# Performance work log

Hardware: AMD Instinct MI355X
Metric: run time of the kernel (lower is better)

The kernel has to match this reference:

```python
import jax, jax.numpy as jnp
import numpy as np

NUM_HEADS = 16

def setup_inputs() -> dict:
    key = jax.random.key(0)
    ks = jax.random.split(key, 11)
    B, S, D = 4, 1024, 1024
    M = 128
    hd = D // NUM_HEADS
    s = 0.02
    return {
        'x':  jax.random.normal(ks[0], (B, S, D), jnp.float32),
        'Wq': jax.random.normal(ks[1], (D, D), jnp.float32) * s,
        'bq': jax.random.normal(ks[2], (D,), jnp.float32) * s,
        'Wk': jax.random.normal(ks[3], (D, D), jnp.float32) * s,
        'bk': jax.random.normal(ks[4], (D,), jnp.float32) * s,
        'Wv': jax.random.normal(ks[5], (D, D), jnp.float32) * s,
        'bv': jax.random.normal(ks[6], (D,), jnp.float32) * s,
        'Wo': jax.random.normal(ks[7], (D, D), jnp.float32) * s,
        'bo': jax.random.normal(ks[8], (D,), jnp.float32) * s,
        'rel_k': jax.random.normal(ks[9], (2 * M + 1, hd), jnp.float32),
        'rel_v': jax.random.normal(ks[10], (2 * M + 1, hd), jnp.float32),
    }

def reference(x, Wq, bq, Wk, bk, Wv, bv, Wo, bo, rel_k, rel_v):
    B, S, D = x.shape
    H = NUM_HEADS
    hd = D // H
    M = (rel_k.shape[0] - 1) // 2

    def proj(W, b):
        # torch nn.Linear: x @ W.T + b, then split heads -> [B,H,S,hd]
        return (x @ W.T + b).reshape(B, S, H, hd).transpose(0, 2, 1, 3)

    q = proj(Wq, bq)
    k = proj(Wk, bk)
    v = proj(Wv, bv)

    # relative position index matrix [S,S]: clip(j - i, -M, M) + M
    r = jnp.arange(S)
    idx = jnp.clip(r[None, :] - r[:, None], -M, M) + M
    rpk = rel_k[idx]  # [S,S,hd] (equivalent to one-hot matmul lookup)
    rpv = rel_v[idx]  # [S,S,hd]

    content = jnp.einsum('bhqd,bhkd->bhqk', q, k)
    relative = jnp.einsum('bhqd,qkd->bhqk', q, rpk)
    scores = (content + relative) / jnp.sqrt(jnp.float32(hd))
    w = jax.nn.softmax(scores, axis=-1)  # [B,H,S,S]

    out = jnp.einsum('bhqk,bhkd->bhqd', w, v) + jnp.einsum('bhqk,qkd->bhqd', w, rpv)
    out = out.transpose(0, 2, 1, 3).reshape(B, S, D)
    return out @ Wo.T + bo
```

## Files before the change

### kernel.cpp

```cpp
#include <hip/hip_runtime.h>
#include <hip/hip_bf16.h>
#include <math.h>

#define SEQ 1024
#define NH 16
#define HD 64
#define DM 1024
#define MWIN 128
#define RR 257

typedef __attribute__((ext_vector_type(8))) short bf16x8;
typedef __attribute__((ext_vector_type(4))) float f32x4;

__device__ __forceinline__ unsigned short f2b_bits(float f) {
  return __builtin_bit_cast(unsigned short, __float2bfloat16(f));
}
__device__ __forceinline__ float b2f(unsigned short u) {
  return __uint_as_float(((unsigned int)u) << 16);
}
__device__ __forceinline__ void gl16(const void* g, void* l) {
  __builtin_amdgcn_global_load_lds(
      (const __attribute__((address_space(1))) unsigned int*)g,
      (__attribute__((address_space(3))) unsigned int*)l, 16, 0, 0);
}

__global__ __launch_bounds__(256) void prep_conv(const float* __restrict__ x,
                                                 const float* __restrict__ w0,
                                                 const float* __restrict__ w1,
                                                 const float* __restrict__ w2,
                                                 const float* __restrict__ w3,
                                                 const float* __restrict__ rk,
                                                 const float* __restrict__ rv,
                                                 unsigned short* __restrict__ xb,
                                                 unsigned short* __restrict__ wb,
                                                 unsigned short* __restrict__ relkb,
                                                 unsigned short* __restrict__ relvtb) {
  const int bid = blockIdx.x, t = threadIdx.x;
  if (bid < 4096) {
    int i = bid * 256 + t;
    float4 v = ((const float4*)x)[i];
    ushort4 o;
    o.x = f2b_bits(v.x); o.y = f2b_bits(v.y); o.z = f2b_bits(v.z); o.w = f2b_bits(v.w);
    ((ushort4*)xb)[i] = o;
  } else if (bid < 8192) {
    int idx = (bid - 4096) * 256 + t;
    const int m = idx >> 18, local = idx & 262143;
    const float* src = m == 0 ? w0 : (m == 1 ? w1 : (m == 2 ? w2 : w3));
    float4 v = ((const float4*)src)[local];
    ushort4 o;
    o.x = f2b_bits(v.x); o.y = f2b_bits(v.y); o.z = f2b_bits(v.z); o.w = f2b_bits(v.w);
    ((ushort4*)wb)[idx] = o;
  } else if (bid < 8288) {
    int idx = (bid - 8192) * 256 + t;
    int r = idx >> 6;
    int rs = r > 256 ? 256 : r;
    relkb[idx] = f2b_bits(rk[rs * HD + (idx & 63)]);
  } else {
    int idx = (bid - 8288) * 256 + t;
    if (idx < 64 * 288) {
      int d = idx / 288, r = idx % 288;
      relvtb[idx] = (r < RR) ? f2b_bits(rv[(size_t)r * HD + d]) : (unsigned short)0;
    }
  }
}

__global__ __launch_bounds__(256) void qkv_gemm(const unsigned short* __restrict__ A,
                                                const unsigned short* __restrict__ Bw,
                                                const float* __restrict__ bq,
                                                const float* __restrict__ bk,
                                                const float* __restrict__ bv,
                                                unsigned short* __restrict__ Qo,
                                                unsigned short* __restrict__ Ko,
                                                unsigned short* __restrict__ Vo) {
  __shared__ unsigned short As[128 * 32];
  __shared__ unsigned short Bs[128 * 32];
  const int t = threadIdx.x;
  const int lane = t & 63;
  const int wave = t >> 6;
  const int wr = wave >> 1, wc = wave & 1;
  const int lrow = lane & 15, lk = lane >> 4;
  const int m0 = blockIdx.x * 128, n0 = blockIdx.y * 128;

  const int mat = n0 >> 10;
  const float* bias = mat == 0 ? bq : (mat == 1 ? bk : bv);
  unsigned short* Co = mat == 0 ? Qo : (mat == 1 ? Ko : Vo);
  const float scale = mat == 0 ? 0.125f : 1.0f;

  const unsigned short* Ag = A + (size_t)m0 * DM;
  const unsigned short* Bg = Bw + (size_t)n0 * DM;
  const int r0 = t >> 2, r1 = (t + 256) >> 2;
  const int c0 = (t & 3) << 3;

  f32x4 acc[4][4] = {};

  for (int k0 = 0; k0 < DM; k0 += 32) {
    __syncthreads();
    gl16(Ag + (size_t)r0 * DM + k0 + c0, &As[t * 8]);
    gl16(Bg + (size_t)r0 * DM + k0 + c0, &Bs[t * 8]);
    gl16(Ag + (size_t)r1 * DM + k0 + c0, &As[(t + 256) * 8]);
    gl16(Bg + (size_t)r1 * DM + k0 + c0, &Bs[(t + 256) * 8]);
    __syncthreads();
    bf16x8 af[4], bfr[4];
#pragma unroll
    for (int i = 0; i < 4; ++i)
      af[i] = *(const bf16x8*)&As[(wr * 64 + i * 16 + lrow) * 32 + lk * 8];
#pragma unroll
    for (int j = 0; j < 4; ++j)
      bfr[j] = *(const bf16x8*)&Bs[(wc * 64 + j * 16 + lrow) * 32 + lk * 8];
#pragma unroll
    for (int i = 0; i < 4; ++i)
#pragma unroll
      for (int j = 0; j < 4; ++j)
        acc[i][j] = __builtin_amdgcn_mfma_f32_16x16x32_bf16(af[i], bfr[j], acc[i][j], 0, 0, 0);
  }

  float bvv[4];
#pragma unroll
  for (int j = 0; j < 4; ++j) bvv[j] = bias[(n0 & 1023) + wc * 64 + j * 16 + lrow];

#pragma unroll
  for (int i = 0; i < 4; ++i) {
#pragma unroll
    for (int j = 0; j < 4; ++j) {
      const int nl = (n0 & 1023) + wc * 64 + j * 16 + lrow;
      const int h = nl >> 6, d = nl & 63;
#pragma unroll
      for (int r = 0; r < 4; ++r) {
        const int m = m0 + wr * 64 + i * 16 + lk * 4 + r;
        const int b = m >> 10, s = m & 1023;
        float v = (acc[i][j][r] + bvv[j]) * scale;
        Co[((size_t)(b * NH + h) * SEQ + s) * HD + d] = f2b_bits(v);
      }
    }
  }
}

template<int MODE>
__global__ __launch_bounds__(256) void mfma_gemm(const unsigned short* __restrict__ A,
                                                 const unsigned short* __restrict__ B,
                                                 const float* __restrict__ bias,
                                                 float* __restrict__ Cf,
                                                 unsigned short* __restrict__ Cb,
                                                 int K) {
  __shared__ unsigned short As[128 * 32];
  __shared__ unsigned short Bs[128 * 32];
  const int t = threadIdx.x;
  const int lane = t & 63;
  const int wave = t >> 6;
  const int wr = wave >> 1, wc = wave & 1;
  const int lrow = lane & 15, lk = lane >> 4;
  const int m0 = blockIdx.x * 128, n0 = blockIdx.y * 128;

  const unsigned short* Ag = A + (size_t)m0 * K;
  const unsigned short* Bg = B + (size_t)n0 * K;
  const int r0 = t >> 2, r1 = (t + 256) >> 2;
  const int c0 = (t & 3) << 3;

  f32x4 acc[4][4] = {};

  for (int k0 = 0; k0 < K; k0 += 32) {
    __syncthreads();
    gl16(Ag + (size_t)r0 * K + k0 + c0, &As[t * 8]);
    gl16(Bg + (size_t)r0 * K + k0 + c0, &Bs[t * 8]);
    gl16(Ag + (size_t)r1 * K + k0 + c0, &As[(t + 256) * 8]);
    gl16(Bg + (size_t)r1 * K + k0 + c0, &Bs[(t + 256) * 8]);
    __syncthreads();
    bf16x8 af[4], bfr[4];
#pragma unroll
    for (int i = 0; i < 4; ++i)
      af[i] = *(const bf16x8*)&As[(wr * 64 + i * 16 + lrow) * 32 + lk * 8];
#pragma unroll
    for (int j = 0; j < 4; ++j)
      bfr[j] = *(const bf16x8*)&Bs[(wc * 64 + j * 16 + lrow) * 32 + lk * 8];
#pragma unroll
    for (int i = 0; i < 4; ++i)
#pragma unroll
      for (int j = 0; j < 4; ++j)
        acc[i][j] = __builtin_amdgcn_mfma_f32_16x16x32_bf16(af[i], bfr[j], acc[i][j], 0, 0, 0);
  }

  float bvv[4];
  if (MODE == 1) {
#pragma unroll
    for (int j = 0; j < 4; ++j) bvv[j] = bias[n0 + wc * 64 + j * 16 + lrow];
  }
#pragma unroll
  for (int i = 0; i < 4; ++i) {
#pragma unroll
    for (int j = 0; j < 4; ++j) {
      const int n = n0 + wc * 64 + j * 16 + lrow;
#pragma unroll
      for (int r = 0; r < 4; ++r) {
        const int m = m0 + wr * 64 + i * 16 + lk * 4 + r;
        float v = acc[i][j][r];
        if (MODE == 1) {
          Cf[(size_t)m * DM + n] = v + bvv[j];
        } else {
          if (n < RR) Cb[(size_t)m * RR + n] = f2b_bits(v);
        }
      }
    }
  }
}

#define FLASH_LDS_BYTES 126976

__global__ __launch_bounds__(512) void flash_mfma(
    const unsigned short* __restrict__ Qb,
    const unsigned short* __restrict__ Kb,
    const unsigned short* __restrict__ Vb,
    const unsigned short* __restrict__ qrb,
    const unsigned short* __restrict__ relvT,
    unsigned short* __restrict__ attnb) {
  extern __shared__ char smem[];
  unsigned short* Ks = (unsigned short*)smem;
  unsigned short (*VT)[144]    = (unsigned short(*)[144])(smem + 16384);
  unsigned short (*Ps)[16][72] = (unsigned short(*)[16][72])(smem + 34816);
  unsigned short (*wrs)[288]   = (unsigned short(*)[288])(smem + 53248);

  const int t = threadIdx.x;
  const int lane = t & 63;
  const int w = t >> 6;
  const int lq = lane & 15;
  const int g  = lane >> 4;
  const int bh = blockIdx.y;
  const int q0 = blockIdx.x * 128;
  const int qw0 = q0 + w * 16;

  const unsigned short* Qp = Qb + (size_t)bh * SEQ * HD;
  const unsigned short* Kp = Kb + (size_t)bh * SEQ * HD;
  const unsigned short* Vp = Vb + (size_t)bh * SEQ * HD;

  {
    unsigned int* wz = (unsigned int*)(smem + 53248);
    for (int i = t; i < 18432; i += 512) wz[i] = 0u;
  }

  bf16x8 aq[2];
  aq[0] = *(const bf16x8*)(Qp + (size_t)(qw0 + lq) * HD + g * 8);
  aq[1] = *(const bf16x8*)(Qp + (size_t)(qw0 + lq) * HD + 32 + g * 8);

  const size_t qrow0 = ((size_t)bh * SEQ + qw0 + g * 4) * RR;
  float bq0[4], bq256[4];
#pragma unroll
  for (int rr = 0; rr < 4; ++rr) {
    bq0[rr]   = b2f(qrb[qrow0 + (size_t)rr * RR]);
    bq256[rr] = b2f(qrb[qrow0 + (size_t)rr * RR + 256]);
  }

  float l[4] = {}, accL[4] = {}, accR[4] = {};
  f32x4 out1[4] = {};

  const int sv = 2 * lane;
  const int dvv = w * 8;
  bf16x8 v00 = *(const bf16x8*)(Vp + (size_t)sv * HD + dvv);
  bf16x8 v10 = *(const bf16x8*)(Vp + (size_t)(sv + 1) * HD + dvv);

  for (int kt = 0; kt < 8; ++kt) {
    const int k0 = kt * 128;
    __syncthreads();

#pragma unroll
    for (int u = 0; u < 2; ++u) {
      const int ch = t + u * 512;
      const int row = ch >> 3;
      const int src = (row << 3) | ((ch & 7) ^ (row & 7));
      gl16(Kp + (size_t)k0 * HD + src * 8, &Ks[ch * 8]);
    }
#pragma unroll
    for (int j = 0; j < 8; ++j) {
      *(unsigned int*)&VT[dvv + j][sv] =
          (unsigned short)v00[j] | ((unsigned int)(unsigned short)v10[j] << 16);
    }

    const int dh0 = k0 - qw0, dh1 = dh0 + 64;
    const int cls0 = dh0 <= -192 ? 0 : (dh0 >= 144 ? 1 : 2);
    const int cls1 = dh1 <= -192 ? 0 : (dh1 >= 144 ? 1 : 2);
    float bias0[4][4], bias1[4][4];
    if (cls0 == 2) {
      const int dbase = dh0 + lq - g * 4;
#pragma unroll
      for (int j = 0; j < 4; ++j)
#pragma unroll
        for (int rr = 0; rr < 4; ++rr) {
          int delta = dbase + j * 16 - rr;
          int r = delta < -MWIN ? 0 : (delta > MWIN ? 256 : delta + MWIN);
          bias0[j][rr] = b2f(qrb[qrow0 + (size_t)rr * RR + r]);
        }
    }
    if (cls1 == 2) {
      const int dbase = dh1 + lq - g * 4;
#pragma unroll
      for (int j = 0; j < 4; ++j)
#pragma unroll
        for (int rr = 0; rr < 4; ++rr) {
          int delta = dbase + j * 16 - rr;
          int r = delta < -MWIN ? 0 : (delta > MWIN ? 256 : delta + MWIN);
          bias1[j][rr] = b2f(qrb[qrow0 + (size_t)rr * RR + r]);
        }
    }
    __syncthreads();

    if (kt < 7) {
      const unsigned short* Vn = Vp + (size_t)(k0 + 128) * HD + dvv;
      v00 = *(const bf16x8*)(Vn + (size_t)sv * HD);
      v10 = *(const bf16x8*)(Vn + (size_t)(sv + 1) * HD);
    }

#pragma unroll
    for (int h = 0; h < 2; ++h) {
      const int dh = h == 0 ? dh0 : dh1;
      const int cls = h == 0 ? cls0 : cls1;
      const float (*bias)[4] = h == 0 ? bias0 : bias1;

      f32x4 sc[4] = {};
#pragma unroll
      for (int j = 0; j < 4; ++j) {
        const int row = h * 64 + j * 16 + lq;
#pragma unroll
        for (int kk = 0; kk < 2; ++kk) {
          const int ch = (kk * 4 + g) ^ (lq & 7);
          bf16x8 bk = *(const bf16x8*)&Ks[row * 64 + ch * 8];
          sc[j] = __builtin_amdgcn_mfma_f32_16x16x32_bf16(aq[kk], bk, sc[j], 0, 0, 0);
        }
      }

      float wvf[4][4], ssum[4] = {};
      if (cls == 2) {
#pragma unroll
        for (int j = 0; j < 4; ++j)
#pragma unroll
          for (int rr = 0; rr < 4; ++rr) {
            float wv = __expf(sc[j][rr] + bias[j][rr]);
            wvf[j][rr] = wv; ssum[rr] += wv;
          }
        const int dbase = dh + lq - g * 4;
#pragma unroll
        for (int j = 0; j < 4; ++j)
#pragma unroll
          for (int rr = 0; rr < 4; ++rr) {
            const unsigned short ub = f2b_bits(wvf[j][rr]);
            Ps[w][g * 4 + rr][j * 16 + lq] = ub;
            const int delta = dbase + j * 16 - rr;
            if (delta <= -MWIN)      accL[rr] += wvf[j][rr];
            else if (delta >= MWIN)  accR[rr] += wvf[j][rr];
            else                     wrs[w * 16 + g * 4 + rr][delta + MWIN] = ub;
          }
      } else {
        const float* bb = cls == 0 ? bq0 : bq256;
#pragma unroll
        for (int j = 0; j < 4; ++j)
#pragma unroll
          for (int rr = 0; rr < 4; ++rr) {
            float wv = __expf(sc[j][rr] + bb[rr]);
            wvf[j][rr] = wv; ssum[rr] += wv;
            Ps[w][g * 4 + rr][j * 16 + lq] = f2b_bits(wv);
          }
#pragma unroll
        for (int rr = 0; rr < 4; ++rr) {
          if (cls == 0) accL[rr] += ssum[rr]; else accR[rr] += ssum[rr];
        }
      }

#pragma unroll
      for (int rr = 0; rr < 4; ++rr) {
        float s0 = ssum[rr];
#pragma unroll
        for (int o = 1; o < 16; o <<= 1) s0 += __shfl_xor(s0, o);
        l[rr] += s0;
      }

      bf16x8 pa[2];
      pa[0] = *(const bf16x8*)&Ps[w][lq][g * 8];
      pa[1] = *(const bf16x8*)&Ps[w][lq][32 + g * 8];
#pragma unroll
      for (int jd = 0; jd < 4; ++jd) {
        const int vrow = jd * 16 + lq;
#pragma unroll
        for (int kk = 0; kk < 2; ++kk) {
          bf16x8 vb = *(const bf16x8*)&VT[vrow][h * 64 + kk * 32 + g * 8];
          out1[jd] = __builtin_amdgcn_mfma_f32_16x16x32_bf16(pa[kk], vb, out1[jd], 0, 0, 0);
        }
      }
    }
  }

#pragma unroll
  for (int rr = 0; rr < 4; ++rr) {
    float sL = accL[rr], sR = accR[rr];
#pragma unroll
    for (int o = 1; o < 16; o <<= 1) { sL += __shfl_xor(sL, o); sR += __shfl_xor(sR, o); }
    if (lq == 0) {
      wrs[w * 16 + g * 4 + rr][0]   = f2b_bits(sL);
      wrs[w * 16 + g * 4 + rr][256] = f2b_bits(sR);
    }
  }
  __syncthreads();

  f32x4 out2[4] = {};
#pragma unroll
  for (int kk = 0; kk < 9; ++kk) {
    bf16x8 pa2 = *(const bf16x8*)&wrs[w * 16 + lq][kk * 32 + g * 8];
#pragma unroll
    for (int jd = 0; jd < 4; ++jd) {
      bf16x8 vb = *(const bf16x8*)(relvT + (size_t)(jd * 16 + lq) * 288 + kk * 32 + g * 8);
      out2[jd] = __builtin_amdgcn_mfma_f32_16x16x32_bf16(pa2, vb, out2[jd], 0, 0, 0);
    }
  }

  const int b = bh >> 4, h = bh & 15;
#pragma unroll
  for (int jd = 0; jd < 4; ++jd)
#pragma unroll
    for (int rr = 0; rr < 4; ++rr) {
      const int s = qw0 + g * 4 + rr;
      const int d = jd * 16 + lq;
      float vout = (out1[jd][rr] + out2[jd][rr]) / l[rr];
      attnb[(size_t)(b * SEQ + s) * DM + h * HD + d] = f2b_bits(vout);
    }
}

extern "C" void kernel_launch(void* const* d_in, const int* in_sizes, int n_in,
                              void* d_out, int out_size, void* d_ws, size_t ws_size,
                              hipStream_t stream) {
  const float* x     = (const float*)d_in[0];
  const float* Wq    = (const float*)d_in[1];
  const float* bq    = (const float*)d_in[2];
  const float* Wk    = (const float*)d_in[3];
  const float* bk    = (const float*)d_in[4];
  const float* Wv    = (const float*)d_in[5];
  const float* bv    = (const float*)d_in[6];
  const float* Wo    = (const float*)d_in[7];
  const float* bo    = (const float*)d_in[8];
  const float* rel_k = (const float*)d_in[9];
  const float* rel_v = (const float*)d_in[10];
  float* out = (float*)d_out;

  unsigned short* us    = (unsigned short*)d_ws;
  unsigned short* qrb   = us;
  unsigned short* xb    = us + 16842752;
  unsigned short* attnb = xb;
  unsigned short* Wqb   = xb + 4194304;
  unsigned short* Wob   = Wqb + 3145728;
  unsigned short* Qbf   = Wob + 1048576;
  unsigned short* Kbb   = Qbf + 4194304;
  unsigned short* Vbb   = Kbb + 4194304;
  unsigned short* relkb = Vbb + 4194304;
  unsigned short* relvtb= relkb + 24576;

  prep_conv<<<8360, 256, 0, stream>>>(x, Wq, Wk, Wv, Wo, rel_k, rel_v,
                                      xb, Wqb, relkb, relvtb);

  qkv_gemm<<<dim3(32, 24), 256, 0, stream>>>(xb, Wqb, bq, bk, bv, Qbf, Kbb, Vbb);

  mfma_gemm<2><<<dim3(512, 3), 256, 0, stream>>>(Qbf, relkb, nullptr, nullptr, qrb, HD);

  (void)hipFuncSetAttribute(reinterpret_cast<const void*>(flash_mfma),
                            hipFuncAttributeMaxDynamicSharedMemorySize,
                            FLASH_LDS_BYTES);
  flash_mfma<<<dim3(8, 64), 512, FLASH_LDS_BYTES, stream>>>(Qbf, Kbb, Vbb, qrb, relvtb, attnb);

  mfma_gemm<1><<<dim3(32, 8), 256, 0, stream>>>(attnb, Wob, bo, out, nullptr, DM);
}
```

Baseline: 240.9 us.

## Prefetch relative bias one tile ahead, compute row sums via MFMA, remap blocks to XCDs

The flash attention kernel now gathers the relative-position bias values for the next key tile one iteration ahead into a double-buffered register array, so their global latency overlaps with the current tile's compute. The per-row softmax denominator is no longer reduced with 16-lane shuffles; it is accumulated by an extra MFMA of the probability tile against a vector of ones. Blocks are remapped so each XCD handles a contiguous group of heads, which is meant to improve L2 reuse of K/V. The final normalisation uses a reciprocal multiply instead of division. The trade-off is higher register pressure from full unrolling and the prefetch buffers, plus row sums that now come from the bf16-rounded probabilities.

```diff
diff --git a/kernel.cpp b/kernel.cpp
--- a/kernel.cpp
+++ b/kernel.cpp
@@ -205,6 +205,29 @@
 
 #define FLASH_LDS_BYTES 126976
 
+#define GATHER(KT, BUF)                                                        \
+  {                                                                            \
+    const int dg0 = (KT) * 128 - qw0, dg1 = dg0 + 64;                          \
+    if (dg0 > -192 && dg0 < 144) {                                             \
+      const int dbase = dg0 + lq - g * 4;                                      \
+      _Pragma("unroll") for (int j = 0; j < 4; ++j)                            \
+      _Pragma("unroll") for (int rr = 0; rr < 4; ++rr) {                       \
+        int delta = dbase + j * 16 - rr;                                       \
+        int r = delta < -MWIN ? 0 : (delta > MWIN ? 256 : delta + MWIN);       \
+        nb[BUF][0][j][rr] = qrb[qrow0 + (size_t)rr * RR + r];                  \
+      }                                                                        \
+    }                                                                          \
+    if (dg1 > -192 && dg1 < 144) {                                             \
+      const int dbase = dg1 + lq - g * 4;                                      \
+      _Pragma("unroll") for (int j = 0; j < 4; ++j)                            \
+      _Pragma("unroll") for (int rr = 0; rr < 4; ++rr) {                       \
+        int delta = dbase + j * 16 - rr;                                       \
+        int r = delta < -MWIN ? 0 : (delta > MWIN ? 256 : delta + MWIN);       \
+        nb[BUF][1][j][rr] = qrb[qrow0 + (size_t)rr * RR + r];                  \
+      }                                                                        \
+    }                                                                          \
+  }
+
 __global__ __launch_bounds__(512) void flash_mfma(
     const unsigned short* __restrict__ Qb,
     const unsigned short* __restrict__ Kb,
@@ -223,8 +246,11 @@
   const int w = t >> 6;
   const int lq = lane & 15;
   const int g  = lane >> 4;
-  const int bh = blockIdx.y;
-  const int q0 = blockIdx.x * 128;
+
+  const int id  = blockIdx.x + blockIdx.y * 8;
+  const int xcd = id & 7, j2 = id >> 3;
+  const int bh  = xcd * 8 + (j2 & 7);
+  const int q0  = (j2 >> 3) * 128;
   const int qw0 = q0 + w * 16;
 
   const unsigned short* Qp = Qb + (size_t)bh * SEQ * HD;
@@ -248,14 +274,22 @@
     bq256[rr] = b2f(qrb[qrow0 + (size_t)rr * RR + 256]);
   }
 
-  float l[4] = {}, accL[4] = {}, accR[4] = {};
-  f32x4 out1[4] = {};
+  bf16x8 vone;
+#pragma unroll
+  for (int i = 0; i < 8; ++i) vone[i] = (short)0x3F80;
+
+  float accL[4] = {}, accR[4] = {};
+  f32x4 out1[4] = {}, lacc = {};
 
   const int sv = 2 * lane;
   const int dvv = w * 8;
   bf16x8 v00 = *(const bf16x8*)(Vp + (size_t)sv * HD + dvv);
   bf16x8 v10 = *(const bf16x8*)(Vp + (size_t)(sv + 1) * HD + dvv);
 
+  unsigned short nb[2][2][4][4];
+  GATHER(0, 0);
+
+#pragma unroll
   for (int kt = 0; kt < 8; ++kt) {
     const int k0 = kt * 128;
     __syncthreads();
@@ -272,46 +306,19 @@
       *(unsigned int*)&VT[dvv + j][sv] =
           (unsigned short)v00[j] | ((unsigned int)(unsigned short)v10[j] << 16);
     }
-
-    const int dh0 = k0 - qw0, dh1 = dh0 + 64;
-    const int cls0 = dh0 <= -192 ? 0 : (dh0 >= 144 ? 1 : 2);
-    const int cls1 = dh1 <= -192 ? 0 : (dh1 >= 144 ? 1 : 2);
-    float bias0[4][4], bias1[4][4];
-    if (cls0 == 2) {
-      const int dbase = dh0 + lq - g * 4;
-#pragma unroll
-      for (int j = 0; j < 4; ++j)
-#pragma unroll
-        for (int rr = 0; rr < 4; ++rr) {
-          int delta = dbase + j * 16 - rr;
-          int r = delta < -MWIN ? 0 : (delta > MWIN ? 256 : delta + MWIN);
-          bias0[j][rr] = b2f(qrb[qrow0 + (size_t)rr * RR + r]);
-        }
-    }
-    if (cls1 == 2) {
-      const int dbase = dh1 + lq - g * 4;
-#pragma unroll
-      for (int j = 0; j < 4; ++j)
-#pragma unroll
-        for (int rr = 0; rr < 4; ++rr) {
-          int delta = dbase + j * 16 - rr;
-          int r = delta < -MWIN ? 0 : (delta > MWIN ? 256 : delta + MWIN);
-          bias1[j][rr] = b2f(qrb[qrow0 + (size_t)rr * RR + r]);
-        }
-    }
     __syncthreads();
 
     if (kt < 7) {
       const unsigned short* Vn = Vp + (size_t)(k0 + 128) * HD + dvv;
       v00 = *(const bf16x8*)(Vn + (size_t)sv * HD);
       v10 = *(const bf16x8*)(Vn + (size_t)(sv + 1) * HD);
+      GATHER(kt + 1, (kt + 1) & 1);
     }
 
 #pragma unroll
     for (int h = 0; h < 2; ++h) {
-      const int dh = h == 0 ? dh0 : dh1;
-      const int cls = h == 0 ? cls0 : cls1;
-      const float (*bias)[4] = h == 0 ? bias0 : bias1;
+      const int dh = k0 - qw0 + h * 64;
+      const int cls = dh <= -192 ? 0 : (dh >= 144 ? 1 : 2);
 
       f32x4 sc[4] = {};
 #pragma unroll
@@ -325,54 +332,45 @@
         }
       }
 
-      float wvf[4][4], ssum[4] = {};
       if (cls == 2) {
+        const int dbase = dh + lq - g * 4;
 #pragma unroll
         for (int j = 0; j < 4; ++j)
 #pragma unroll
           for (int rr = 0; rr < 4; ++rr) {
-            float wv = __expf(sc[j][rr] + bias[j][rr]);
-            wvf[j][rr] = wv; ssum[rr] += wv;
-          }
-        const int dbase = dh + lq - g * 4;
-#pragma unroll
-        for (int j = 0; j < 4; ++j)
-#pragma unroll
-          for (int rr = 0; rr < 4; ++rr) {
-            const unsigned short ub = f2b_bits(wvf[j][rr]);
+            float wv = __expf(sc[j][rr] + b2f(nb[kt & 1][h][j][rr]));
+            const unsigned short ub = f2b_bits(wv);
             Ps[w][g * 4 + rr][j * 16 + lq] = ub;
             const int delta = dbase + j * 16 - rr;
-            if (delta <= -MWIN)      accL[rr] += wvf[j][rr];
-            else if (delta >= MWIN)  accR[rr] += wvf[j][rr];
+            if (delta <= -MWIN)      accL[rr] += wv;
+            else if (delta >= MWIN)  accR[rr] += wv;
             else                     wrs[w * 16 + g * 4 + rr][delta + MWIN] = ub;
           }
       } else {
-        const float* bb = cls == 0 ? bq0 : bq256;
+        float ts[4] = {};
 #pragma unroll
         for (int j = 0; j < 4; ++j)
 #pragma unroll
           for (int rr = 0; rr < 4; ++rr) {
-            float wv = __expf(sc[j][rr] + bb[rr]);
-            wvf[j][rr] = wv; ssum[rr] += wv;
+            float bb = cls == 0 ? bq0[rr] : bq256[rr];
+            float wv = __expf(sc[j][rr] + bb);
+            ts[rr] += wv;
             Ps[w][g * 4 + rr][j * 16 + lq] = f2b_bits(wv);
           }
-#pragma unroll
-        for (int rr = 0; rr < 4; ++rr) {
-          if (cls == 0) accL[rr] += ssum[rr]; else accR[rr] += ssum[rr];
+        if (cls == 0) {
+#pragma unroll
+          for (int rr = 0; rr < 4; ++rr) accL[rr] += ts[rr];
+        } else {
+#pragma unroll
+          for (int rr = 0; rr < 4; ++rr) accR[rr] += ts[rr];
         }
-      }
-
-#pragma unroll
-      for (int rr = 0; rr < 4; ++rr) {
-        float s0 = ssum[rr];
-#pragma unroll
-        for (int o = 1; o < 16; o <<= 1) s0 += __shfl_xor(s0, o);
-        l[rr] += s0;
       }
 
       bf16x8 pa[2];
       pa[0] = *(const bf16x8*)&Ps[w][lq][g * 8];
       pa[1] = *(const bf16x8*)&Ps[w][lq][32 + g * 8];
+      lacc = __builtin_amdgcn_mfma_f32_16x16x32_bf16(pa[0], vone, lacc, 0, 0, 0);
+      lacc = __builtin_amdgcn_mfma_f32_16x16x32_bf16(pa[1], vone, lacc, 0, 0, 0);
 #pragma unroll
       for (int jd = 0; jd < 4; ++jd) {
         const int vrow = jd * 16 + lq;
@@ -410,14 +408,16 @@
 
   const int b = bh >> 4, h = bh & 15;
 #pragma unroll
-  for (int jd = 0; jd < 4; ++jd)
-#pragma unroll
-    for (int rr = 0; rr < 4; ++rr) {
-      const int s = qw0 + g * 4 + rr;
+  for (int rr = 0; rr < 4; ++rr) {
+    const float inv = 1.0f / lacc[rr];
+    const int s = qw0 + g * 4 + rr;
+#pragma unroll
+    for (int jd = 0; jd < 4; ++jd) {
       const int d = jd * 16 + lq;
-      float vout = (out1[jd][rr] + out2[jd][rr]) / l[rr];
+      float vout = (out1[jd][rr] + out2[jd][rr]) * inv;
       attnb[(size_t)(b * SEQ + s) * DM + h * HD + d] = f2b_bits(vout);
     }
+  }
 }
 
 extern "C" void kernel_launch(void* const* d_in, const int* in_sizes, int n_in,
```

Result: faster. 233.3 us (-3.2%).
